# Kernel tuning notes

Measured on AMD Instinct MI355X. Metric: run time of the kernel, lower is better.

The kernel has to match this reference:

```python
import jax, jax.numpy as jnp
import numpy as np
from jax import lax

BN_EPS = 1e-5


def ternary_quantize(x):
    # thresholds from global max/min, split range into thirds
    mx, mn = jnp.max(x), jnp.min(x)
    lo = mn + (mx - mn) / 3
    hi = mx - (mx - mn) / 3
    return jnp.where(x < lo, -1.0, jnp.where(x > hi, 1.0, 0.0)).astype(x.dtype)


def noised_tri_conv(x, w):
    # w: [O, I, 3, 3]; bias=False in BasicBlock
    tw = w - jnp.mean(w)
    tq = ternary_quantize(tw)
    out = lax.conv_general_dilated(
        x, tq, window_strides=(1, 1), padding=((1, 1), (1, 1)),
        dimension_numbers=('NCHW', 'OIHW', 'NCHW'))
    # noised_forward: per-pixel conv of a 1x1 patch with padding=1 ->
    # only the center tap of the 3x3 kernel contributes; generated noise
    # weights are unused in the original code (faithful reproduction);
    # result is detached in torch.
    center = tq[:, :, 1, 1]  # [O, I]
    extra = lax.stop_gradient(jnp.einsum('bchw,oc->bohw', x, center))
    return out + extra


def batch_norm_train(x, gamma, beta):
    mean = jnp.mean(x, axis=(0, 2, 3), keepdims=True)
    var = jnp.var(x, axis=(0, 2, 3), keepdims=True)  # biased, as torch BN
    xhat = (x - mean) * lax.rsqrt(var + BN_EPS)
    return xhat * gamma[None, :, None, None] + beta[None, :, None, None]


def setup_inputs() -> dict:
    key = jax.random.key(0)
    k = jax.random.split(key, 7)
    C = 256
    x = jax.random.normal(k[0], (16, C, 56, 56), dtype=jnp.float32)
    w1 = jax.random.normal(k[1], (C, C, 3, 3), dtype=jnp.float32) * 0.05
    w2 = jax.random.normal(k[2], (C, C, 3, 3), dtype=jnp.float32) * 0.05
    g1 = jax.random.uniform(k[3], (C,), dtype=jnp.float32, minval=0.5, maxval=1.5)
    b1 = jax.random.normal(k[4], (C,), dtype=jnp.float32) * 0.1
    g2 = jax.random.uniform(k[5], (C,), dtype=jnp.float32, minval=0.5, maxval=1.5)
    b2 = jax.random.normal(k[6], (C,), dtype=jnp.float32) * 0.1
    return {'x': x, 'w1': w1, 'w2': w2, 'g1': g1, 'b1': b1, 'g2': g2, 'b2': b2}


def reference(x, w1, w2, g1, b1, g2, b2):
    out1 = noised_tri_conv(x, w1)
    out1 = batch_norm_train(out1, g1, b1)
    out1 = jax.nn.relu(out1)
    out2 = noised_tri_conv(out1, w2)
    out2 = batch_norm_train(out2, g2, b2)
    return jax.nn.relu(out1 + out2)
```

## Files before the change

kernel.cpp:

```cpp
#include <hip/hip_runtime.h>

typedef __bf16 bf16;
typedef __bf16 bf16x8 __attribute__((ext_vector_type(8)));
typedef float f32x4 __attribute__((ext_vector_type(4)));

#define NIMG 16
#define CCH 256
#define HH 56
#define HP 58
#define NBLK (NIMG * 14)
#define NPART 896
#define NPOSV (NIMG * HH * HH)
#define WELEMS 589824

typedef const __attribute__((address_space(1))) void* gas1_t;
typedef __attribute__((address_space(3))) void* las3_t;

__device__ __forceinline__ void gload16(const void* g, void* l) {
  __builtin_amdgcn_global_load_lds((gas1_t)g, (las3_t)l, 16, 0, 0);
}


__global__ __launch_bounds__(256) void w_partial(const float* __restrict__ w1,
                                                 const float* __restrict__ w2,
                                                 double* __restrict__ psum,
                                                 float* __restrict__ pmn,
                                                 float* __restrict__ pmx) {
  int b = blockIdx.x;
  int lb = b & 127;
  const float* w = (b >> 7) ? w2 : w1;
  int t = threadIdx.x;
  double s = 0.0;
  float mn = 3.4028235e38f, mx = -3.4028235e38f;
  for (int i = lb * 4608 + t; i < (lb + 1) * 4608; i += 256) {
    float v = w[i];
    s += (double)v;
    mn = fminf(mn, v);
    mx = fmaxf(mx, v);
  }
  __shared__ double sd[256];
  __shared__ float smn[256], smx[256];
  sd[t] = s; smn[t] = mn; smx[t] = mx;
  __syncthreads();
  for (int st = 128; st > 0; st >>= 1) {
    if (t < st) {
      sd[t] += sd[t + st];
      smn[t] = fminf(smn[t], smn[t + st]);
      smx[t] = fmaxf(smx[t], smx[t + st]);
    }
    __syncthreads();
  }
  if (t == 0) { psum[b] = sd[0]; pmn[b] = smn[0]; pmx[b] = smx[0]; }
}

__global__ void w_finalize(const double* __restrict__ psum,
                           const float* __restrict__ pmn,
                           const float* __restrict__ pmx,
                           float* __restrict__ wq) {
  int t = threadIdx.x;
  if (t < 2) {
    double s = 0.0;
    float mn = 3.4028235e38f, mx = -3.4028235e38f;
    for (int b = t * 128; b < (t + 1) * 128; b++) {
      s += psum[b];
      mn = fminf(mn, pmn[b]);
      mx = fmaxf(mx, pmx[b]);
    }
    float mean = (float)(s / (double)WELEMS);
    float tmn = mn - mean, tmx = mx - mean;
    float d = (tmx - tmn) / 3.0f;
    wq[t * 4 + 0] = mean;
    wq[t * 4 + 1] = tmn + d;
    wq[t * 4 + 2] = tmx - d;
  }
}

__global__ __launch_bounds__(256) void w_quant(const float* __restrict__ w1,
                                               const float* __restrict__ w2,
                                               const float* __restrict__ wq,
                                               bf16* __restrict__ btf1,
                                               bf16* __restrict__ btf2) {
  int bid = blockIdx.x;
  int widx = bid / 2304;
  const float* w = widx ? w2 : w1;
  bf16* bt = widx ? btf2 : btf1;
  float mean = wq[widx * 4], lo = wq[widx * 4 + 1], hi = wq[widx * 4 + 2];
  int e = (bid % 2304) * 256 + threadIdx.x;
  int ki = e & 7;
  int l = (e >> 3) & 63;
  int frag = e >> 9;
  int ob = frag & 15;
  int rest = frag >> 4;
  int kk = rest & 1;
  int scc = rest >> 1;
  int cc = scc & 3;
  int s = scc >> 2;
  int o = ob * 16 + (l & 15);
  int c = cc * 64 + kk * 32 + (l >> 4) * 8 + ki;
  float tv = w[(size_t)o * 2304 + c * 9 + s] - mean;
  float q = tv < lo ? -1.f : (tv > hi ? 1.f : 0.f);
  if (s == 4) q *= 2.f;
  bt[e] = (bf16)q;
}

__global__ __launch_bounds__(256) void pad_convert(const float* __restrict__ x,
                                                   bf16* __restrict__ xpad) {
  int bid = blockIdx.x;
  int hp = bid % HP;
  int n = bid / HP;
  int t = threadIdx.x;
  bf16* orow = xpad + (size_t)(n * HP + hp) * HP * CCH;
  bf16x8 z;
#pragma unroll
  for (int q = 0; q < 8; ++q) z[q] = (bf16)0.f;
  if (hp == 0 || hp == HP - 1) {
    for (int j = t; j < HP * 32; j += 256)
      *(bf16x8*)(orow + (size_t)(j >> 5) * CCH + (j & 31) * 8) = z;
    return;
  }
  __shared__ float tile[CCH * 57];
  const float* xb = x + (size_t)n * CCH * (HH * HH) + (size_t)(hp - 1) * HH;
  for (int j = t; j < CCH * 14; j += 256) {
    int c = j / 14, wq = j % 14;
    float4 v = *(const float4*)(xb + (size_t)c * (HH * HH) + wq * 4);
    float* tp = &tile[c * 57 + wq * 4];
    tp[0] = v.x; tp[1] = v.y; tp[2] = v.z; tp[3] = v.w;
  }
  __syncthreads();
  const int cg = t & 31;
  for (int j = t; j < HP * 32; j += 256) {
    int wp = j >> 5;
    bf16x8 ov = z;
    if (wp >= 1 && wp <= HH) {
#pragma unroll
      for (int q = 0; q < 8; ++q) ov[q] = (bf16)tile[(cg * 8 + q) * 57 + (wp - 1)];
    }
    *(bf16x8*)(orow + (size_t)wp * CCH + cg * 8) = ov;
  }
}

template <int MODE>
__global__ __launch_bounds__(512, 2) void conv_gemm(const bf16* __restrict__ xpad,
                                                    const bf16* __restrict__ btf,
                                                    float* __restrict__ part,
                                                    const bf16* __restrict__ v1pad,
                                                    const float* __restrict__ bnp,
                                                    float* __restrict__ outf,
                                                    bf16* __restrict__ outb) {
  __shared__ __align__(16) char smem[116736];
  const int t = threadIdx.x;
  const int lane = t & 63, wv = t >> 6;
  const int wm = wv >> 2, wn = wv & 3;
  const int g = lane >> 4, li = lane & 15;
  const int rawbid = blockIdx.x;
  const int bid = (rawbid & 7) * (NBLK / 8) + (rawbid >> 3);
  const int n = bid / 14, h0 = (bid % 14) * 4;

  f32x4 acc[8][4];
#pragma unroll
  for (int i = 0; i < 8; i++)
#pragma unroll
    for (int j = 0; j < 4; j++) acc[i][j] = f32x4{0.f, 0.f, 0.f, 0.f};

  auto stageA = [&](int cc, int b) {
#pragma unroll
    for (int i = 0; i < 6; ++i) {
      int idx = wv + i * 8;
      int rr = idx >> 3, po = idx & 7;
      int pp = po * 8 + (lane >> 3);
      int gs = (lane & 7) ^ (lane >> 3);
      const bf16* src = xpad + ((size_t)(n * HP + h0 + rr) * HP + pp) * CCH + cc * 64 + gs * 8;
      gload16(src, smem + b * 49152 + rr * 8192 + po * 1024 + lane * 16);
    }
  };

  auto loadB = [&](bf16x8 (&dst)[4], int s, int cc, int kk) {
#pragma unroll
    for (int f = 0; f < 4; ++f) {
      size_t fragidx = (size_t)(((s * 4 + cc) * 2 + kk) * 16 + wn * 4 + f);
      dst[f] = *(const bf16x8*)(btf + fragidx * 512 + lane * 8);
    }
  };

  auto compute_half = [&](const char* Ab, int half, int dh, int dw, int kk,
                          const bf16x8 (&bx)[4]) {
    bf16x8 a[4];
    int rr = 2 * wm + half + dh;
#pragma unroll
    for (int pc = 0; pc < 4; ++pc) {
      int p = pc * 16 + li + dw;
      int sl = (kk * 4 + g) ^ (p & 7);
      a[pc] = *(const bf16x8*)(Ab + rr * 8192 + p * 128 + sl * 16);
    }
#pragma unroll
    for (int pc = 0; pc < 4; ++pc)
#pragma unroll
      for (int fn = 0; fn < 4; ++fn)
        acc[half * 4 + pc][fn] =
          __builtin_amdgcn_mfma_f32_16x16x32_bf16(a[pc], bx[fn], acc[half * 4 + pc][fn], 0, 0, 0);
  };

  stageA(0, 0);
  bf16x8 bS[2][4];
  bf16x8 bB[4];
  loadB(bS[0], 0, 0, 0);
  __syncthreads();

#pragma unroll
  for (int cc = 0; cc < 4; ++cc) {
    const char* Ab = smem + (cc & 1) * 49152;
    if (cc < 3) stageA(cc + 1, (cc + 1) & 1);
#pragma unroll
    for (int s = 0; s < 9; ++s) {
      const int dh = s / 3, dw = s % 3;
      const int cur = (cc * 9 + s) & 1, nxt = cur ^ 1;
      if (s < 8) loadB(bS[nxt], s + 1, cc, 0);
      else if (cc < 3) loadB(bS[nxt], 0, cc + 1, 0);
      loadB(bB, s, cc, 1);
      __builtin_amdgcn_sched_barrier(0);
      __builtin_amdgcn_s_setprio(1);
      compute_half(Ab, 0, dh, dw, 0, bS[cur]);
      compute_half(Ab, 1, dh, dw, 0, bS[cur]);
      compute_half(Ab, 0, dh, dw, 1, bB);
      compute_half(Ab, 1, dh, dw, 1, bB);
      __builtin_amdgcn_s_setprio(0);
    }
    __syncthreads();
  }

  if (MODE == 1 || MODE == 3) {
    float so[2][4] = {{0.f,0.f,0.f,0.f},{0.f,0.f,0.f,0.f}};
    float qo[2][4] = {{0.f,0.f,0.f,0.f},{0.f,0.f,0.f,0.f}};
#pragma unroll
    for (int fm = 0; fm < 8; ++fm) {
      const int rl = fm >> 2, pc = fm & 3;
      const size_t rowoff = (size_t)(n * HH + h0 + 2 * wm + rl) * HH * CCH;
#pragma unroll
      for (int r = 0; r < 4; ++r) {
        int w = pc * 16 + g * 4 + r;
        if (w < HH) {
#pragma unroll
          for (int fn = 0; fn < 4; ++fn) {
            float v = acc[fm][fn][r];
            so[rl][fn] += v;
            qo[rl][fn] += v * v;
            if (MODE == 3) outb[rowoff + (size_t)w * CCH + wn * 64 + fn * 16 + li] = (bf16)v;
          }
        }
      }
    }
#pragma unroll
    for (int rl = 0; rl < 2; ++rl)
#pragma unroll
      for (int fn = 0; fn < 4; ++fn) {
        so[rl][fn] += __shfl_xor(so[rl][fn], 16);
        so[rl][fn] += __shfl_xor(so[rl][fn], 32);
        qo[rl][fn] += __shfl_xor(qo[rl][fn], 16);
        qo[rl][fn] += __shfl_xor(qo[rl][fn], 32);
      }
    if (g == 0) {
#pragma unroll
      for (int rl = 0; rl < 2; ++rl)
#pragma unroll
        for (int fn = 0; fn < 4; ++fn) {
          int o = wn * 64 + fn * 16 + lane;
          size_t prow = (size_t)(bid * 4 + 2 * wm + rl);
          part[(prow * CCH + o) * 2 + 0] = so[rl][fn];
          part[(prow * CCH + o) * 2 + 1] = qo[rl][fn];
        }
    }
  } else {
    float sc[4], bi[4];
#pragma unroll
    for (int fn = 0; fn < 4; ++fn) {
      int o = wn * 64 + fn * 16 + li;
      sc[fn] = bnp[o * 2];
      bi[fn] = bnp[o * 2 + 1];
    }
    float* fsm = (float*)smem;
    const int TS = 3648;
    for (int rl = 0; rl < 2; ++rl) {
      __syncthreads();
      const int row = h0 + 2 * wm + rl;
#pragma unroll
      for (int pc = 0; pc < 4; ++pc) {
        const int fm = rl * 4 + pc;
#pragma unroll
        for (int r = 0; r < 4; ++r) {
          int w = pc * 16 + g * 4 + r;
          if (w < HH) {
#pragma unroll
            for (int fn = 0; fn < 4; ++fn) {
              int o_loc = fn * 16 + li;
              fsm[wv * TS + w * 65 + o_loc] = acc[fm][fn][r] * sc[fn] + bi[fn];
            }
          }
        }
      }
      const bf16* v1row = v1pad + ((size_t)(n * HP + row + 1) * HP + 1) * CCH + wn * 64;
      for (int i = lane; i < HH * 8; i += 64) {
        int w = i >> 3, og = i & 7;
        bf16x8 v1v = *(const bf16x8*)(v1row + (size_t)w * CCH + og * 8);
        float* tp = &fsm[wv * TS + w * 65 + og * 8];
#pragma unroll
        for (int q = 0; q < 8; ++q) {
          float v = tp[q] + (float)v1v[q];
          tp[q] = v > 0.f ? v : 0.f;
        }
      }
      __syncthreads();
#pragma unroll
      for (int tl = 0; tl < 8; ++tl) {
        int wmt = tl >> 2, wnt = tl & 3;
        int orow = h0 + 2 * wmt + rl;
        for (int j = t; j < 4096; j += 512) {
          int oo = j >> 6, w = j & 63;
          if (w < HH)
            outf[(((size_t)n * CCH + wnt * 64 + oo) * HH + orow) * HH + w] = fsm[tl * TS + w * 65 + oo];
        }
      }
    }
  }
}

__global__ __launch_bounds__(256) void fuse2(const bf16* __restrict__ raw,
                                             const bf16* __restrict__ v1pad,
                                             const float* __restrict__ bnp,
                                             float* __restrict__ out) {
  __shared__ float tile[CCH * 57];
  int bid = blockIdx.x;
  int n = bid / HH, h = bid % HH;
  int t = threadIdx.x;
  const bf16* rrow = raw + (size_t)(n * HH + h) * HH * CCH;
  const bf16* vrow = v1pad + ((size_t)(n * HP + h + 1) * HP + 1) * CCH;
  const int cg = t & 31;
  float sc[8], bi[8];
#pragma unroll
  for (int q = 0; q < 8; ++q) {
    sc[q] = bnp[(cg * 8 + q) * 2];
    bi[q] = bnp[(cg * 8 + q) * 2 + 1];
  }
  for (int j = t; j < HH * 32; j += 256) {
    int w = j >> 5;
    bf16x8 r8 = *(const bf16x8*)(rrow + (size_t)w * CCH + cg * 8);
    bf16x8 v8 = *(const bf16x8*)(vrow + (size_t)w * CCH + cg * 8);
#pragma unroll
    for (int q = 0; q < 8; ++q) {
      float v = (float)r8[q] * sc[q] + bi[q] + (float)v8[q];
      tile[(cg * 8 + q) * 57 + w] = v > 0.f ? v : 0.f;
    }
  }
  __syncthreads();
  float* ob = out + (size_t)n * CCH * (HH * HH) + (size_t)h * HH;
  for (int j = t; j < CCH * 14; j += 256) {
    int c = j / 14, wq = j % 14;
    const float* tp = &tile[c * 57 + wq * 4];
    float4 v = {tp[0], tp[1], tp[2], tp[3]};
    *(float4*)(ob + (size_t)c * (HH * HH) + wq * 4) = v;
  }
}

__global__ __launch_bounds__(256) void bn_reduce1(const float* __restrict__ part,
                                                  float* __restrict__ part2) {
  int t = threadIdx.x, b = blockIdx.x;
  float s = 0.f, q = 0.f;
  for (int r = b * 28; r < (b + 1) * 28; r++) {
    s += part[((size_t)r * CCH + t) * 2 + 0];
    q += part[((size_t)r * CCH + t) * 2 + 1];
  }
  part2[((size_t)b * CCH + t) * 2 + 0] = s;
  part2[((size_t)b * CCH + t) * 2 + 1] = q;
}

__global__ __launch_bounds__(256) void bn_reduce2(const float* __restrict__ part2,
                                                  const float* __restrict__ gamma,
                                                  const float* __restrict__ beta,
                                                  float* __restrict__ params) {
  int t = threadIdx.x;
  float s = 0.f, q = 0.f;
  for (int b = 0; b < 32; b++) {
    s += part2[((size_t)b * CCH + t) * 2 + 0];
    q += part2[((size_t)b * CCH + t) * 2 + 1];
  }
  const float inv = 1.f / (float)NPOSV;
  float mean = s * inv;
  float var = q * inv - mean * mean;
  float sc = gamma[t] / sqrtf(var + 1e-5f);
  params[t * 2 + 0] = sc;
  params[t * 2 + 1] = beta[t] - mean * sc;
}

__global__ __launch_bounds__(256) void bn_apply_b(const bf16* __restrict__ rawb,
                                                  const float* __restrict__ params,
                                                  bf16* __restrict__ xpad) {
  int bid = blockIdx.x;
  int hp = bid % HP;
  int n = bid / HP;
  int t = threadIdx.x;
  bf16* orow = xpad + (size_t)(n * HP + hp) * HP * CCH;
  bf16x8 z;
#pragma unroll
  for (int q = 0; q < 8; ++q) z[q] = (bf16)0.f;
  if (hp == 0 || hp == HP - 1) {
    for (int j = t; j < HP * 32; j += 256)
      *(bf16x8*)(orow + (size_t)(j >> 5) * CCH + (j & 31) * 8) = z;
    return;
  }
  const int cg = t & 31, ws8 = t >> 5;
  float sc[8], bi[8];
#pragma unroll
  for (int q = 0; q < 8; ++q) {
    sc[q] = params[(cg * 8 + q) * 2];
    bi[q] = params[(cg * 8 + q) * 2 + 1];
  }
  const bf16* rrow = rawb + (size_t)(n * HH + (hp - 1)) * HH * CCH;
  for (int wp = ws8; wp < HP; wp += 8) {
    bf16x8 ov = z;
    if (wp >= 1 && wp <= HH) {
      bf16x8 r8 = *(const bf16x8*)(rrow + (size_t)(wp - 1) * CCH + cg * 8);
#pragma unroll
      for (int q = 0; q < 8; ++q) {
        float v = (float)r8[q] * sc[q] + bi[q];
        ov[q] = (bf16)(v > 0.f ? v : 0.f);
      }
    }
    *(bf16x8*)(orow + (size_t)wp * CCH + cg * 8) = ov;
  }
}


extern "C" void kernel_launch(void* const* d_in, const int* in_sizes, int n_in,
                              void* d_out, int out_size, void* d_ws, size_t ws_size,
                              hipStream_t stream) {
  const float* x  = (const float*)d_in[0];
  const float* w1 = (const float*)d_in[1];
  const float* w2 = (const float*)d_in[2];
  const float* g1 = (const float*)d_in[3];
  const float* b1 = (const float*)d_in[4];
  const float* g2 = (const float*)d_in[5];
  const float* b2 = (const float*)d_in[6];
  float* out = (float*)d_out;
  char* ws = (char*)d_ws;

  constexpr size_t O_BT1  = 0;
  constexpr size_t O_BT2  = O_BT1 + 1179648;
  constexpr size_t O_XPAD = O_BT2 + 1179648;
  constexpr size_t O_PART = O_XPAD + (size_t)NIMG * HP * HP * CCH * 2 + 65536;
  constexpr size_t O_PSUM = O_PART + (size_t)NPART * CCH * 2 * 4;
  constexpr size_t O_PMN  = O_PSUM + 2048;
  constexpr size_t O_PMX  = O_PMN + 1024;
  constexpr size_t O_WQ   = O_PMX + 1024;
  constexpr size_t O_BNP1 = O_WQ + 256;
  constexpr size_t O_BNP2 = O_BNP1 + 2048;
  constexpr size_t O_PART2 = O_BNP2 + 2048;
  constexpr size_t O_OUT2RAW = O_PART2 + 65536;
  constexpr size_t NEED_BIG = O_OUT2RAW + (size_t)NPOSV * CCH * 2 + 65536;

  bf16* bt1 = (bf16*)(ws + O_BT1);
  bf16* bt2 = (bf16*)(ws + O_BT2);
  bf16* xpad = (bf16*)(ws + O_XPAD);
  bf16* out1pad = (bf16*)(ws + O_XPAD);
  float* part = (float*)(ws + O_PART);
  double* psum = (double*)(ws + O_PSUM);
  float* pmn = (float*)(ws + O_PMN);
  float* pmx = (float*)(ws + O_PMX);
  float* wq = (float*)(ws + O_WQ);
  float* bnp1 = (float*)(ws + O_BNP1);
  float* bnp2 = (float*)(ws + O_BNP2);
  float* part2 = (float*)(ws + O_PART2);
  bf16* out2raw = (bf16*)(ws + O_OUT2RAW);
  bf16* out1rawb = (bf16*)d_out;

  w_partial<<<256, 256, 0, stream>>>(w1, w2, psum, pmn, pmx);
  w_finalize<<<1, 64, 0, stream>>>(psum, pmn, pmx, wq);
  w_quant<<<4608, 256, 0, stream>>>(w1, w2, wq, bt1, bt2);
  pad_convert<<<NIMG * HP, 256, 0, stream>>>(x, xpad);
  conv_gemm<3><<<NBLK, 512, 0, stream>>>(xpad, bt1, part, nullptr, nullptr, nullptr, out1rawb);
  bn_reduce1<<<32, 256, 0, stream>>>(part, part2);
  bn_reduce2<<<1, 256, 0, stream>>>(part2, g1, b1, bnp1);
  bn_apply_b<<<NIMG * HP, 256, 0, stream>>>(out1rawb, bnp1, out1pad);
  if (ws_size >= NEED_BIG) {
    conv_gemm<3><<<NBLK, 512, 0, stream>>>(out1pad, bt2, part, nullptr, nullptr, nullptr, out2raw);
    bn_reduce1<<<32, 256, 0, stream>>>(part, part2);
    bn_reduce2<<<1, 256, 0, stream>>>(part2, g2, b2, bnp2);
    fuse2<<<NIMG * HH, 256, 0, stream>>>(out2raw, out1pad, bnp2, out);
  } else {
    conv_gemm<1><<<NBLK, 512, 0, stream>>>(out1pad, bt2, part, nullptr, nullptr, nullptr, nullptr);
    bn_reduce1<<<32, 256, 0, stream>>>(part, part2);
    bn_reduce2<<<1, 256, 0, stream>>>(part2, g2, b2, bnp2);
    conv_gemm<2><<<NBLK, 512, 0, stream>>>(out1pad, bt2, nullptr, out1pad, bnp2, out, nullptr);
  }
}
```

Baseline: 192.0 us.

## Fuse small setup and BN-reduce kernels to cut launch count

Merges the weight-statistics partial reduction and the pad/convert pass into one pre_kernel, folds the weight finalize step into w_quant (each block re-reduces 128 partials), and merges the two-stage BN reduction into one kernel using an atomic last-block ticket. The fallback low-workspace path and the MODE-templated conv epilogues are removed, so the big-workspace path always runs. This removes several tiny kernel launches and their serialization gaps. In exchange it adds redundant per-block reduction work in w_quant and needs the atomic counter reset, and it drops the workspace-size check.

```diff
diff --git a/kernel.cpp b/kernel.cpp
--- a/kernel.cpp
+++ b/kernel.cpp
@@ -12,6 +12,7 @@
 #define NPART 896
 #define NPOSV (NIMG * HH * HH)
 #define WELEMS 589824
+#define NPADB (NIMG * HP)
 
 typedef const __attribute__((address_space(1))) void* gas1_t;
 typedef __attribute__((address_space(3))) void* las3_t;
@@ -20,72 +21,125 @@
   __builtin_amdgcn_global_load_lds((gas1_t)g, (las3_t)l, 16, 0, 0);
 }
 
-
-__global__ __launch_bounds__(256) void w_partial(const float* __restrict__ w1,
-                                                 const float* __restrict__ w2,
-                                                 double* __restrict__ psum,
-                                                 float* __restrict__ pmn,
-                                                 float* __restrict__ pmx) {
-  int b = blockIdx.x;
-  int lb = b & 127;
-  const float* w = (b >> 7) ? w2 : w1;
-  int t = threadIdx.x;
-  double s = 0.0;
-  float mn = 3.4028235e38f, mx = -3.4028235e38f;
-  for (int i = lb * 4608 + t; i < (lb + 1) * 4608; i += 256) {
-    float v = w[i];
-    s += (double)v;
-    mn = fminf(mn, v);
-    mx = fmaxf(mx, v);
-  }
-  __shared__ double sd[256];
-  __shared__ float smn[256], smx[256];
-  sd[t] = s; smn[t] = mn; smx[t] = mx;
-  __syncthreads();
-  for (int st = 128; st > 0; st >>= 1) {
-    if (t < st) {
-      sd[t] += sd[t + st];
-      smn[t] = fminf(smn[t], smn[t + st]);
-      smx[t] = fmaxf(smx[t], smx[t + st]);
-    }
-    __syncthreads();
-  }
-  if (t == 0) { psum[b] = sd[0]; pmn[b] = smn[0]; pmx[b] = smx[0]; }
-}
-
-__global__ void w_finalize(const double* __restrict__ psum,
-                           const float* __restrict__ pmn,
-                           const float* __restrict__ pmx,
-                           float* __restrict__ wq) {
-  int t = threadIdx.x;
-  if (t < 2) {
+__global__ __launch_bounds__(256) void pre_kernel(const float* __restrict__ x,
+                                                  bf16* __restrict__ xpad,
+                                                  const float* __restrict__ w1,
+                                                  const float* __restrict__ w2,
+                                                  double* __restrict__ psum,
+                                                  float* __restrict__ pmn,
+                                                  float* __restrict__ pmx,
+                                                  unsigned* __restrict__ cnt) {
+  __shared__ __align__(16) char sm[58368];
+  const int blk = blockIdx.x;
+  const int t = threadIdx.x;
+
+  if (blk >= NPADB + 256) {
+    if (t < 8) cnt[t] = 0u;
+    return;
+  }
+
+  if (blk >= NPADB) {
+    int b = blk - NPADB;
+    int lb = b & 127;
+    const float* w = (b >> 7) ? w2 : w1;
     double s = 0.0;
     float mn = 3.4028235e38f, mx = -3.4028235e38f;
-    for (int b = t * 128; b < (t + 1) * 128; b++) {
-      s += psum[b];
-      mn = fminf(mn, pmn[b]);
-      mx = fmaxf(mx, pmx[b]);
-    }
-    float mean = (float)(s / (double)WELEMS);
-    float tmn = mn - mean, tmx = mx - mean;
-    float d = (tmx - tmn) / 3.0f;
-    wq[t * 4 + 0] = mean;
-    wq[t * 4 + 1] = tmn + d;
-    wq[t * 4 + 2] = tmx - d;
+    for (int i = lb * 4608 + t; i < (lb + 1) * 4608; i += 256) {
+      float v = w[i];
+      s += (double)v;
+      mn = fminf(mn, v);
+      mx = fmaxf(mx, v);
+    }
+    double* sd = (double*)sm;
+    float* smn = (float*)(sm + 2048);
+    float* smx = (float*)(sm + 3072);
+    sd[t] = s; smn[t] = mn; smx[t] = mx;
+    __syncthreads();
+    for (int st = 128; st > 0; st >>= 1) {
+      if (t < st) {
+        sd[t] += sd[t + st];
+        smn[t] = fminf(smn[t], smn[t + st]);
+        smx[t] = fmaxf(smx[t], smx[t + st]);
+      }
+      __syncthreads();
+    }
+    if (t == 0) { psum[b] = sd[0]; pmn[b] = smn[0]; pmx[b] = smx[0]; }
+    return;
+  }
+
+  int hp = blk % HP;
+  int n = blk / HP;
+  bf16* orow = xpad + (size_t)(n * HP + hp) * HP * CCH;
+  bf16x8 z;
+#pragma unroll
+  for (int q = 0; q < 8; ++q) z[q] = (bf16)0.f;
+  if (hp == 0 || hp == HP - 1) {
+    for (int j = t; j < HP * 32; j += 256)
+      *(bf16x8*)(orow + (size_t)(j >> 5) * CCH + (j & 31) * 8) = z;
+    return;
+  }
+  float* tile = (float*)sm;
+  const float* xb = x + (size_t)n * CCH * (HH * HH) + (size_t)(hp - 1) * HH;
+  for (int j = t; j < CCH * 14; j += 256) {
+    int c = j / 14, wq = j % 14;
+    float4 v = *(const float4*)(xb + (size_t)c * (HH * HH) + wq * 4);
+    float* tp = &tile[c * 57 + wq * 4];
+    tp[0] = v.x; tp[1] = v.y; tp[2] = v.z; tp[3] = v.w;
+  }
+  __syncthreads();
+  const int cg = t & 31;
+  for (int j = t; j < HP * 32; j += 256) {
+    int wp = j >> 5;
+    bf16x8 ov = z;
+    if (wp >= 1 && wp <= HH) {
+#pragma unroll
+      for (int q = 0; q < 8; ++q) ov[q] = (bf16)tile[(cg * 8 + q) * 57 + (wp - 1)];
+    }
+    *(bf16x8*)(orow + (size_t)wp * CCH + cg * 8) = ov;
   }
 }
 
 __global__ __launch_bounds__(256) void w_quant(const float* __restrict__ w1,
                                                const float* __restrict__ w2,
-                                               const float* __restrict__ wq,
+                                               const double* __restrict__ psum,
+                                               const float* __restrict__ pmn,
+                                               const float* __restrict__ pmx,
                                                bf16* __restrict__ btf1,
                                                bf16* __restrict__ btf2) {
   int bid = blockIdx.x;
   int widx = bid / 2304;
   const float* w = widx ? w2 : w1;
   bf16* bt = widx ? btf2 : btf1;
-  float mean = wq[widx * 4], lo = wq[widx * 4 + 1], hi = wq[widx * 4 + 2];
-  int e = (bid % 2304) * 256 + threadIdx.x;
+  int t = threadIdx.x;
+  __shared__ double sd[128];
+  __shared__ float smn[128], smx[128];
+  __shared__ float s_mean, s_lo, s_hi;
+  if (t < 128) {
+    sd[t] = psum[widx * 128 + t];
+    smn[t] = pmn[widx * 128 + t];
+    smx[t] = pmx[widx * 128 + t];
+  }
+  __syncthreads();
+  for (int st = 64; st > 0; st >>= 1) {
+    if (t < st) {
+      sd[t] += sd[t + st];
+      smn[t] = fminf(smn[t], smn[t + st]);
+      smx[t] = fmaxf(smx[t], smx[t + st]);
+    }
+    __syncthreads();
+  }
+  if (t == 0) {
+    float mean = (float)(sd[0] / (double)WELEMS);
+    float tmn = smn[0] - mean, tmx = smx[0] - mean;
+    float d = (tmx - tmn) / 3.0f;
+    s_mean = mean;
+    s_lo = tmn + d;
+    s_hi = tmx - d;
+  }
+  __syncthreads();
+  float mean = s_mean, lo = s_lo, hi = s_hi;
+
+  int e = (bid % 2304) * 256 + t;
   int ki = e & 7;
   int l = (e >> 3) & 63;
   int frag = e >> 9;
@@ -103,51 +157,11 @@
   bt[e] = (bf16)q;
 }
 
-__global__ __launch_bounds__(256) void pad_convert(const float* __restrict__ x,
-                                                   bf16* __restrict__ xpad) {
-  int bid = blockIdx.x;
-  int hp = bid % HP;
-  int n = bid / HP;
-  int t = threadIdx.x;
-  bf16* orow = xpad + (size_t)(n * HP + hp) * HP * CCH;
-  bf16x8 z;
-#pragma unroll
-  for (int q = 0; q < 8; ++q) z[q] = (bf16)0.f;
-  if (hp == 0 || hp == HP - 1) {
-    for (int j = t; j < HP * 32; j += 256)
-      *(bf16x8*)(orow + (size_t)(j >> 5) * CCH + (j & 31) * 8) = z;
-    return;
-  }
-  __shared__ float tile[CCH * 57];
-  const float* xb = x + (size_t)n * CCH * (HH * HH) + (size_t)(hp - 1) * HH;
-  for (int j = t; j < CCH * 14; j += 256) {
-    int c = j / 14, wq = j % 14;
-    float4 v = *(const float4*)(xb + (size_t)c * (HH * HH) + wq * 4);
-    float* tp = &tile[c * 57 + wq * 4];
-    tp[0] = v.x; tp[1] = v.y; tp[2] = v.z; tp[3] = v.w;
-  }
-  __syncthreads();
-  const int cg = t & 31;
-  for (int j = t; j < HP * 32; j += 256) {
-    int wp = j >> 5;
-    bf16x8 ov = z;
-    if (wp >= 1 && wp <= HH) {
-#pragma unroll
-      for (int q = 0; q < 8; ++q) ov[q] = (bf16)tile[(cg * 8 + q) * 57 + (wp - 1)];
-    }
-    *(bf16x8*)(orow + (size_t)wp * CCH + cg * 8) = ov;
-  }
-}
-
-template <int MODE>
 __global__ __launch_bounds__(512, 2) void conv_gemm(const bf16* __restrict__ xpad,
                                                     const bf16* __restrict__ btf,
                                                     float* __restrict__ part,
-                                                    const bf16* __restrict__ v1pad,
-                                                    const float* __restrict__ bnp,
-                                                    float* __restrict__ outf,
                                                     bf16* __restrict__ outb) {
-  __shared__ __align__(16) char smem[116736];
+  __shared__ __align__(16) char smem[98304];
   const int t = threadIdx.x;
   const int lane = t & 63, wv = t >> 6;
   const int wm = wv >> 2, wn = wv & 3;
@@ -228,98 +242,118 @@
     __syncthreads();
   }
 
-  if (MODE == 1 || MODE == 3) {
-    float so[2][4] = {{0.f,0.f,0.f,0.f},{0.f,0.f,0.f,0.f}};
-    float qo[2][4] = {{0.f,0.f,0.f,0.f},{0.f,0.f,0.f,0.f}};
-#pragma unroll
-    for (int fm = 0; fm < 8; ++fm) {
-      const int rl = fm >> 2, pc = fm & 3;
-      const size_t rowoff = (size_t)(n * HH + h0 + 2 * wm + rl) * HH * CCH;
-#pragma unroll
-      for (int r = 0; r < 4; ++r) {
-        int w = pc * 16 + g * 4 + r;
-        if (w < HH) {
-#pragma unroll
-          for (int fn = 0; fn < 4; ++fn) {
-            float v = acc[fm][fn][r];
-            so[rl][fn] += v;
-            qo[rl][fn] += v * v;
-            if (MODE == 3) outb[rowoff + (size_t)w * CCH + wn * 64 + fn * 16 + li] = (bf16)v;
-          }
+  float so[2][4] = {{0.f,0.f,0.f,0.f},{0.f,0.f,0.f,0.f}};
+  float qo[2][4] = {{0.f,0.f,0.f,0.f},{0.f,0.f,0.f,0.f}};
+#pragma unroll
+  for (int fm = 0; fm < 8; ++fm) {
+    const int rl = fm >> 2, pc = fm & 3;
+    const size_t rowoff = (size_t)(n * HH + h0 + 2 * wm + rl) * HH * CCH;
+#pragma unroll
+    for (int r = 0; r < 4; ++r) {
+      int w = pc * 16 + g * 4 + r;
+      if (w < HH) {
+#pragma unroll
+        for (int fn = 0; fn < 4; ++fn) {
+          float v = acc[fm][fn][r];
+          so[rl][fn] += v;
+          qo[rl][fn] += v * v;
+          outb[rowoff + (size_t)w * CCH + wn * 64 + fn * 16 + li] = (bf16)v;
         }
       }
     }
+  }
+#pragma unroll
+  for (int rl = 0; rl < 2; ++rl)
+#pragma unroll
+    for (int fn = 0; fn < 4; ++fn) {
+      so[rl][fn] += __shfl_xor(so[rl][fn], 16);
+      so[rl][fn] += __shfl_xor(so[rl][fn], 32);
+      qo[rl][fn] += __shfl_xor(qo[rl][fn], 16);
+      qo[rl][fn] += __shfl_xor(qo[rl][fn], 32);
+    }
+  if (g == 0) {
 #pragma unroll
     for (int rl = 0; rl < 2; ++rl)
 #pragma unroll
       for (int fn = 0; fn < 4; ++fn) {
-        so[rl][fn] += __shfl_xor(so[rl][fn], 16);
-        so[rl][fn] += __shfl_xor(so[rl][fn], 32);
-        qo[rl][fn] += __shfl_xor(qo[rl][fn], 16);
-        qo[rl][fn] += __shfl_xor(qo[rl][fn], 32);
+        int o = wn * 64 + fn * 16 + lane;
+        size_t prow = (size_t)(bid * 4 + 2 * wm + rl);
+        part[(prow * CCH + o) * 2 + 0] = so[rl][fn];
+        part[(prow * CCH + o) * 2 + 1] = qo[rl][fn];
       }
-    if (g == 0) {
-#pragma unroll
-      for (int rl = 0; rl < 2; ++rl)
-#pragma unroll
-        for (int fn = 0; fn < 4; ++fn) {
-          int o = wn * 64 + fn * 16 + lane;
-          size_t prow = (size_t)(bid * 4 + 2 * wm + rl);
-          part[(prow * CCH + o) * 2 + 0] = so[rl][fn];
-          part[(prow * CCH + o) * 2 + 1] = qo[rl][fn];
-        }
-    }
-  } else {
-    float sc[4], bi[4];
-#pragma unroll
-    for (int fn = 0; fn < 4; ++fn) {
-      int o = wn * 64 + fn * 16 + li;
-      sc[fn] = bnp[o * 2];
-      bi[fn] = bnp[o * 2 + 1];
-    }
-    float* fsm = (float*)smem;
-    const int TS = 3648;
-    for (int rl = 0; rl < 2; ++rl) {
-      __syncthreads();
-      const int row = h0 + 2 * wm + rl;
-#pragma unroll
-      for (int pc = 0; pc < 4; ++pc) {
-        const int fm = rl * 4 + pc;
-#pragma unroll
-        for (int r = 0; r < 4; ++r) {
-          int w = pc * 16 + g * 4 + r;
-          if (w < HH) {
-#pragma unroll
-            for (int fn = 0; fn < 4; ++fn) {
-              int o_loc = fn * 16 + li;
-              fsm[wv * TS + w * 65 + o_loc] = acc[fm][fn][r] * sc[fn] + bi[fn];
-            }
-          }
-        }
+  }
+}
+
+__global__ __launch_bounds__(256) void bn_reduce(const float* __restrict__ part,
+                                                 float* __restrict__ part2,
+                                                 const float* __restrict__ gamma,
+                                                 const float* __restrict__ beta,
+                                                 float* __restrict__ params,
+                                                 unsigned* __restrict__ cnt) {
+  int t = threadIdx.x, b = blockIdx.x;
+  float s = 0.f, q = 0.f;
+  for (int r = b * 28; r < (b + 1) * 28; r++) {
+    s += part[((size_t)r * CCH + t) * 2 + 0];
+    q += part[((size_t)r * CCH + t) * 2 + 1];
+  }
+  part2[((size_t)b * CCH + t) * 2 + 0] = s;
+  part2[((size_t)b * CCH + t) * 2 + 1] = q;
+  __threadfence();
+  __syncthreads();
+  __shared__ unsigned ticket;
+  if (t == 0) ticket = atomicAdd(cnt, 1u);
+  __syncthreads();
+  if (ticket == 31u) {
+    __threadfence();
+    float s2 = 0.f, q2 = 0.f;
+    for (int b2 = 0; b2 < 32; b2++) {
+      s2 += part2[((size_t)b2 * CCH + t) * 2 + 0];
+      q2 += part2[((size_t)b2 * CCH + t) * 2 + 1];
+    }
+    const float inv = 1.f / (float)NPOSV;
+    float mean = s2 * inv;
+    float var = q2 * inv - mean * mean;
+    float sc = gamma[t] / sqrtf(var + 1e-5f);
+    params[t * 2 + 0] = sc;
+    params[t * 2 + 1] = beta[t] - mean * sc;
+  }
+}
+
+__global__ __launch_bounds__(256) void bn_apply_b(const bf16* __restrict__ rawb,
+                                                  const float* __restrict__ params,
+                                                  bf16* __restrict__ xpad) {
+  int bid = blockIdx.x;
+  int hp = bid % HP;
+  int n = bid / HP;
+  int t = threadIdx.x;
+  bf16* orow = xpad + (size_t)(n * HP + hp) * HP * CCH;
+  bf16x8 z;
+#pragma unroll
+  for (int q = 0; q < 8; ++q) z[q] = (bf16)0.f;
+  if (hp == 0 || hp == HP - 1) {
+    for (int j = t; j < HP * 32; j += 256)
+      *(bf16x8*)(orow + (size_t)(j >> 5) * CCH + (j & 31) * 8) = z;
+    return;
+  }
+  const int cg = t & 31, ws8 = t >> 5;
+  float sc[8], bi[8];
+#pragma unroll
+  for (int q = 0; q < 8; ++q) {
+    sc[q] = params[(cg * 8 + q) * 2];
+    bi[q] = params[(cg * 8 + q) * 2 + 1];
+  }
+  const bf16* rrow = rawb + (size_t)(n * HH + (hp - 1)) * HH * CCH;
+  for (int wp = ws8; wp < HP; wp += 8) {
+    bf16x8 ov = z;
+    if (wp >= 1 && wp <= HH) {
+      bf16x8 r8 = *(const bf16x8*)(rrow + (size_t)(wp - 1) * CCH + cg * 8);
+#pragma unroll
+      for (int q = 0; q < 8; ++q) {
+        float v = (float)r8[q] * sc[q] + bi[q];
+        ov[q] = (bf16)(v > 0.f ? v : 0.f);
       }
-      const bf16* v1row = v1pad + ((size_t)(n * HP + row + 1) * HP + 1) * CCH + wn * 64;
-      for (int i = lane; i < HH * 8; i += 64) {
-        int w = i >> 3, og = i & 7;
-        bf16x8 v1v = *(const bf16x8*)(v1row + (size_t)w * CCH + og * 8);
-        float* tp = &fsm[wv * TS + w * 65 + og * 8];
-#pragma unroll
-        for (int q = 0; q < 8; ++q) {
-          float v = tp[q] + (float)v1v[q];
-          tp[q] = v > 0.f ? v : 0.f;
-        }
-      }
-      __syncthreads();
-#pragma unroll
-      for (int tl = 0; tl < 8; ++tl) {
-        int wmt = tl >> 2, wnt = tl & 3;
-        int orow = h0 + 2 * wmt + rl;
-        for (int j = t; j < 4096; j += 512) {
-          int oo = j >> 6, w = j & 63;
-          if (w < HH)
-            outf[(((size_t)n * CCH + wnt * 64 + oo) * HH + orow) * HH + w] = fsm[tl * TS + w * 65 + oo];
-        }
-      }
-    }
+    }
+    *(bf16x8*)(orow + (size_t)wp * CCH + cg * 8) = ov;
   }
 }
 
@@ -360,74 +394,6 @@
   }
 }
 
-__global__ __launch_bounds__(256) void bn_reduce1(const float* __restrict__ part,
-                                                  float* __restrict__ part2) {
-  int t = threadIdx.x, b = blockIdx.x;
-  float s = 0.f, q = 0.f;
-  for (int r = b * 28; r < (b + 1) * 28; r++) {
-    s += part[((size_t)r * CCH + t) * 2 + 0];
-    q += part[((size_t)r * CCH + t) * 2 + 1];
-  }
-  part2[((size_t)b * CCH + t) * 2 + 0] = s;
-  part2[((size_t)b * CCH + t) * 2 + 1] = q;
-}
-
-__global__ __launch_bounds__(256) void bn_reduce2(const float* __restrict__ part2,
-                                                  const float* __restrict__ gamma,
-                                                  const float* __restrict__ beta,
-                                                  float* __restrict__ params) {
-  int t = threadIdx.x;
-  float s = 0.f, q = 0.f;
-  for (int b = 0; b < 32; b++) {
-    s += part2[((size_t)b * CCH + t) * 2 + 0];
-    q += part2[((size_t)b * CCH + t) * 2 + 1];
-  }
-  const float inv = 1.f / (float)NPOSV;
-  float mean = s * inv;
-  float var = q * inv - mean * mean;
-  float sc = gamma[t] / sqrtf(var + 1e-5f);
-  params[t * 2 + 0] = sc;
-  params[t * 2 + 1] = beta[t] - mean * sc;
-}
-
-__global__ __launch_bounds__(256) void bn_apply_b(const bf16* __restrict__ rawb,
-                                                  const float* __restrict__ params,
-                                                  bf16* __restrict__ xpad) {
-  int bid = blockIdx.x;
-  int hp = bid % HP;
-  int n = bid / HP;
-  int t = threadIdx.x;
-  bf16* orow = xpad + (size_t)(n * HP + hp) * HP * CCH;
-  bf16x8 z;
-#pragma unroll
-  for (int q = 0; q < 8; ++q) z[q] = (bf16)0.f;
-  if (hp == 0 || hp == HP - 1) {
-    for (int j = t; j < HP * 32; j += 256)
-      *(bf16x8*)(orow + (size_t)(j >> 5) * CCH + (j & 31) * 8) = z;
-    return;
-  }
-  const int cg = t & 31, ws8 = t >> 5;
-  float sc[8], bi[8];
-#pragma unroll
-  for (int q = 0; q < 8; ++q) {
-    sc[q] = params[(cg * 8 + q) * 2];
-    bi[q] = params[(cg * 8 + q) * 2 + 1];
-  }
-  const bf16* rrow = rawb + (size_t)(n * HH + (hp - 1)) * HH * CCH;
-  for (int wp = ws8; wp < HP; wp += 8) {
-    bf16x8 ov = z;
-    if (wp >= 1 && wp <= HH) {
-      bf16x8 r8 = *(const bf16x8*)(rrow + (size_t)(wp - 1) * CCH + cg * 8);
-#pragma unroll
-      for (int q = 0; q < 8; ++q) {
-        float v = (float)r8[q] * sc[q] + bi[q];
-        ov[q] = (bf16)(v > 0.f ? v : 0.f);
-      }
-    }
-    *(bf16x8*)(orow + (size_t)wp * CCH + cg * 8) = ov;
-  }
-}
-
 
 extern "C" void kernel_launch(void* const* d_in, const int* in_sizes, int n_in,
                               void* d_out, int out_size, void* d_ws, size_t ws_size,
@@ -449,12 +415,11 @@
   constexpr size_t O_PSUM = O_PART + (size_t)NPART * CCH * 2 * 4;
   constexpr size_t O_PMN  = O_PSUM + 2048;
   constexpr size_t O_PMX  = O_PMN + 1024;
-  constexpr size_t O_WQ   = O_PMX + 1024;
-  constexpr size_t O_BNP1 = O_WQ + 256;
+  constexpr size_t O_BNP1 = O_PMX + 1024;
   constexpr size_t O_BNP2 = O_BNP1 + 2048;
   constexpr size_t O_PART2 = O_BNP2 + 2048;
-  constexpr size_t O_OUT2RAW = O_PART2 + 65536;
-  constexpr size_t NEED_BIG = O_OUT2RAW + (size_t)NPOSV * CCH * 2 + 65536;
+  constexpr size_t O_CNT  = O_PART2 + 65536;
+  constexpr size_t O_OUT2RAW = O_CNT + 65536;
 
   bf16* bt1 = (bf16*)(ws + O_BT1);
   bf16* bt2 = (bf16*)(ws + O_BT2);
@@ -464,30 +429,19 @@
   double* psum = (double*)(ws + O_PSUM);
   float* pmn = (float*)(ws + O_PMN);
   float* pmx = (float*)(ws + O_PMX);
-  float* wq = (float*)(ws + O_WQ);
   float* bnp1 = (float*)(ws + O_BNP1);
   float* bnp2 = (float*)(ws + O_BNP2);
   float* part2 = (float*)(ws + O_PART2);
+  unsigned* cnt = (unsigned*)(ws + O_CNT);
   bf16* out2raw = (bf16*)(ws + O_OUT2RAW);
   bf16* out1rawb = (bf16*)d_out;
 
-  w_partial<<<256, 256, 0, stream>>>(w1, w2, psum, pmn, pmx);
-  w_finalize<<<1, 64, 0, stream>>>(psum, pmn, pmx, wq);
-  w_quant<<<4608, 256, 0, stream>>>(w1, w2, wq, bt1, bt2);
-  pad_convert<<<NIMG * HP, 256, 0, stream>>>(x, xpad);
-  conv_gemm<3><<<NBLK, 512, 0, stream>>>(xpad, bt1, part, nullptr, nullptr, nullptr, out1rawb);
-  bn_reduce1<<<32, 256, 0, stream>>>(part, part2);
-  bn_reduce2<<<1, 256, 0, stream>>>(part2, g1, b1, bnp1);
+  pre_kernel<<<NPADB + 256 + 1, 256, 0, stream>>>(x, xpad, w1, w2, psum, pmn, pmx, cnt);
+  w_quant<<<4608, 256, 0, stream>>>(w1, w2, psum, pmn, pmx, bt1, bt2);
+  conv_gemm<<<NBLK, 512, 0, stream>>>(xpad, bt1, part, out1rawb);
+  bn_reduce<<<32, 256, 0, stream>>>(part, part2, g1, b1, bnp1, cnt + 0);
   bn_apply_b<<<NIMG * HP, 256, 0, stream>>>(out1rawb, bnp1, out1pad);
-  if (ws_size >= NEED_BIG) {
-    conv_gemm<3><<<NBLK, 512, 0, stream>>>(out1pad, bt2, part, nullptr, nullptr, nullptr, out2raw);
-    bn_reduce1<<<32, 256, 0, stream>>>(part, part2);
-    bn_reduce2<<<1, 256, 0, stream>>>(part2, g2, b2, bnp2);
-    fuse2<<<NIMG * HH, 256, 0, stream>>>(out2raw, out1pad, bnp2, out);
-  } else {
-    conv_gemm<1><<<NBLK, 512, 0, stream>>>(out1pad, bt2, part, nullptr, nullptr, nullptr, nullptr);
-    bn_reduce1<<<32, 256, 0, stream>>>(part, part2);
-    bn_reduce2<<<1, 256, 0, stream>>>(part2, g2, b2, bnp2);
-    conv_gemm<2><<<NBLK, 512, 0, stream>>>(out1pad, bt2, nullptr, out1pad, bnp2, out, nullptr);
-  }
-}
+  conv_gemm<<<NBLK, 512, 0, stream>>>(out1pad, bt2, part, out2raw);
+  bn_reduce<<<32, 256, 0, stream>>>(part, part2, g2, b2, bnp2, cnt + 1);
+  fuse2<<<NIMG * HH, 256, 0, stream>>>(out2raw, out1pad, bnp2, out);
+}
```

Result: no change. 191.9 us (-0.0%).
